# Kernel tuning notes

Hardware: AMD Instinct MI355X
Metric: run time of the kernel (lower is better)

## Reference

```python
import jax, jax.numpy as jnp
import numpy as np
from jax import lax


def _lstm_last(x, Wih, Whh, bih, bhh):
    """Single-layer torch-style LSTM (gate order i,f,g,o); returns last hidden state.
    x: (M, T, F) -> (M, H)."""
    gx = jnp.einsum('mtf,gf->mtg', x, Wih) + bih + bhh  # precompute input contributions
    H = Whh.shape[1]
    Wh = Whh.T
    def step(carry, g):
        h, c = carry
        z = g + h @ Wh
        i, f, gg, o = jnp.split(z, 4, axis=-1)
        c = jax.nn.sigmoid(f) * c + jax.nn.sigmoid(i) * jnp.tanh(gg)
        h = jax.nn.sigmoid(o) * jnp.tanh(c)
        return (h, c), None
    M = x.shape[0]
    init = (jnp.zeros((M, H), x.dtype), jnp.zeros((M, H), x.dtype))
    (h, _), _ = lax.scan(step, init, jnp.swapaxes(gx, 0, 1))
    return h


def _forward(input_data, rel_encoding, lstm_Wih, lstm_Whh, lstm_bih, lstm_bhh,
             hop_w1, hop_b1, hop_w2, hop_b2, fn_w1, fn_b1, fn_w2, fn_b2):
    B, W, N, F = input_data.shape
    U = lstm_Whh.shape[1]
    # SequentialEmbedding: per-stock LSTM over the window, take last step
    x = jnp.transpose(input_data, (0, 2, 1, 3)).reshape(B * N, W, F)
    seq = _lstm_last(x, lstm_Wih, lstm_Whh, lstm_bih, lstm_bhh).reshape(B, N, U)

    # RelationalEmbedding: dense N x N k-hop message passing
    mask = (rel_encoding.sum(-1) > 0).astype(seq.dtype)  # (N,N)
    D = mask.sum(-1)                                      # (N,) degrees (self-loops keep >0)
    e = seq
    for k in range(hop_w1.shape[0]):  # k_hops: small fixed loop
        W1 = hop_w1[k]
        # mask * concat([e_i, e_j, enc]) @ W1 + b1, computed blockwise without
        # materializing the (B,N,N,2U+K) concat; mask scales only the pre-bias term
        xi = e @ W1[:U]                                    # (B,N,INP)
        xj = e @ W1[U:2 * U]                               # (B,N,INP)
        xe = jnp.einsum('ijk,kp->ijp', rel_encoding, W1[2 * U:])  # (N,N,INP)
        pre = mask[None, :, :, None] * (xi[:, :, None, :] + xj[:, None, :, :] + xe[None]) + hop_b1[k]
        hdn = jax.nn.leaky_relu(pre)                       # (B,N,N,INP)
        wts = jax.nn.leaky_relu(hdn @ hop_w2[k] + hop_b2[k])[..., 0]  # (B,N,N)
        scaled = (wts * mask) / D[None, :, None]
        # torch: sum_i scaled[b,i,j] * e_j  ==  e_j * (sum_i scaled[b,i,j])
        e = scaled.sum(axis=1)[..., None] * e

    # FullyConnected head: Linear(2U,2U)+LeakyReLU, Linear(2U,1)+LeakyReLU, squeeze
    comb = jnp.concatenate([seq, e], axis=-1)              # (B,N,2U)
    out = jax.nn.leaky_relu(comb @ fn_w1 + fn_b1)
    out = jax.nn.leaky_relu(out @ fn_w2 + fn_b2)
    return out[..., 0]                                     # (B,N)


def setup_inputs() -> dict:
    key = jax.random.key(0)
    ks = jax.random.split(key, 14)
    B, W, N, F = 2, 32, 768, 4
    U, K, KH = 32, 8, 2
    INP = 2 * U + K  # 72
    def w(k, shape, fan):
        return jax.random.normal(k, shape, jnp.float32) / np.float32(np.sqrt(fan))
    enc = (jax.random.uniform(ks[1], (N, N, K)) < 0.05).astype(jnp.float32)
    # self-loops in relation channel 0 so every node has degree >= 1
    enc = enc.at[:, :, 0].set(jnp.maximum(enc[:, :, 0], jnp.eye(N, dtype=jnp.float32)))
    return {
        'input_data': jax.random.normal(ks[0], (B, W, N, F), jnp.float32),
        'rel_encoding': enc,
        'lstm_Wih': w(ks[2], (4 * U, F), F),
        'lstm_Whh': w(ks[3], (4 * U, U), U),
        'lstm_bih': 0.01 * jax.random.normal(ks[4], (4 * U,), jnp.float32),
        'lstm_bhh': 0.01 * jax.random.normal(ks[5], (4 * U,), jnp.float32),
        'hop_w1': w(ks[6], (KH, INP, INP), INP),
        'hop_b1': 0.01 * jax.random.normal(ks[7], (KH, INP), jnp.float32),
        'hop_w2': w(ks[8], (KH, INP, 1), INP),
        'hop_b2': 0.01 * jax.random.normal(ks[9], (KH, 1), jnp.float32),
        'fn_w1': w(ks[10], (2 * U, 2 * U), 2 * U),
        'fn_b1': 0.01 * jax.random.normal(ks[11], (2 * U,), jnp.float32),
        'fn_w2': w(ks[12], (2 * U, 1), 2 * U),
        'fn_b2': 0.01 * jax.random.normal(ks[13], (1,), jnp.float32),
    }


def reference(input_data, rel_encoding, lstm_Wih, lstm_Whh, lstm_bih, lstm_bhh,
              hop_w1, hop_b1, hop_w2, hop_b2, fn_w1, fn_b1, fn_w2, fn_b2):
    return _forward(input_data, rel_encoding, lstm_Wih, lstm_Whh, lstm_bih, lstm_bhh,
                    hop_w1, hop_b1, hop_w2, hop_b2, fn_w1, fn_b1, fn_w2, fn_b2)
```

## Files before the change

### kernel.cpp

```cpp
#include <hip/hip_runtime.h>

#define N_STK 768
#define BATCH 2
#define WIN   32
#define FEAT  4
#define UNITS 32
#define INP   72
#define CHUNK 64

__device__ __forceinline__ float lrelu(float v){ return v > 0.0f ? v : 0.01f*v; }
__device__ __forceinline__ float lanebcast(float v, int l){
    return __int_as_float(__builtin_amdgcn_readlane(__float_as_int(v), l));
}
__device__ __forceinline__ unsigned patof(const float* __restrict__ p){
    float4 a = *reinterpret_cast<const float4*>(p);
    float4 b = *reinterpret_cast<const float4*>(p + 4);
    unsigned m = 0;
    m |= (a.x != 0.0f) ? 1u   : 0u;
    m |= (a.y != 0.0f) ? 2u   : 0u;
    m |= (a.z != 0.0f) ? 4u   : 0u;
    m |= (a.w != 0.0f) ? 8u   : 0u;
    m |= (b.x != 0.0f) ? 16u  : 0u;
    m |= (b.y != 0.0f) ? 32u  : 0u;
    m |= (b.z != 0.0f) ? 64u  : 0u;
    m |= (b.w != 0.0f) ? 128u : 0u;
    return m;
}

__global__ __launch_bounds__(256) void k1_kernel(const float* __restrict__ rel,
        const float* __restrict__ x, const float* __restrict__ Wih,
        const float* __restrict__ Whh, const float* __restrict__ bih,
        const float* __restrict__ bhh, const float* __restrict__ hop_w1,
        const float* __restrict__ hop_b1,
        float* __restrict__ seq, float* __restrict__ invD, int* __restrict__ cnt,
        unsigned* __restrict__ list, float* __restrict__ lutlo, float* __restrict__ luthi,
        float* __restrict__ xi0, float* __restrict__ xj0){
    int j = blockIdx.x, tid = threadIdx.x;
    int wv = tid >> 6, lane = tid & 63;
    __shared__ float hrow[2][UNITS];

    if (wv < 2){
        int b = wv;
        int r0 = lane, r1 = 64 + lane;
        bool low = (lane < 32);
        float4 wi0 = *reinterpret_cast<const float4*>(Wih + r0*FEAT);
        float4 wi1 = *reinterpret_cast<const float4*>(Wih + r1*FEAT);
        float bb0 = bih[r0] + bhh[r0];
        float bb1 = bih[r1] + bhh[r1];
        float4 W0[8], W1[8];
        #pragma unroll
        for (int q = 0; q < 8; q++){
            W0[q] = *reinterpret_cast<const float4*>(Whh + r0*UNITS + q*4);
            W1[q] = *reinterpret_cast<const float4*>(Whh + r1*UNITS + q*4);
        }
        float4 xv = make_float4(0.f, 0.f, 0.f, 0.f);
        if (low) xv = *reinterpret_cast<const float4*>(x + ((size_t)(b*WIN + lane)*N_STK + j)*FEAT);
        float hreg = 0.0f, c = 0.0f;
        #pragma unroll 1
        for (int t = 0; t < WIN; t++){
            float xb0 = lanebcast(xv.x, t), xb1 = lanebcast(xv.y, t);
            float xb2 = lanebcast(xv.z, t), xb3 = lanebcast(xv.w, t);
            float z0a = bb0 + wi0.x*xb0 + wi0.z*xb2;
            float z0b =       wi0.y*xb1 + wi0.w*xb3;
            float z1a = bb1 + wi1.x*xb0 + wi1.z*xb2;
            float z1b =       wi1.y*xb1 + wi1.w*xb3;
            #pragma unroll
            for (int q = 0; q < 8; q++){
                float h0 = lanebcast(hreg, 32 + q*4 + 0);
                float h1 = lanebcast(hreg, 32 + q*4 + 1);
                float h2 = lanebcast(hreg, 32 + q*4 + 2);
                float h3 = lanebcast(hreg, 32 + q*4 + 3);
                z0a += W0[q].x*h0; z0b += W0[q].y*h1;
                z0a += W0[q].z*h2; z0b += W0[q].w*h3;
                z1a += W1[q].x*h0; z1b += W1[q].y*h1;
                z1a += W1[q].z*h2; z1b += W1[q].w*h3;
            }
            float z0 = z0a + z0b, z1 = z1a + z1b;
            float e0 = __expf(-z0);
            float s0 = 1.0f/(1.0f + e0);
            float sc = low ? -2.0f : -1.0f;
            float e1 = __expf(sc*z1);
            float rr = 1.0f/(1.0f + e1);
            float act = low ? (1.0f - e1)*rr : rr;
            float pa = s0*act;
            float po = __shfl_xor(pa, 32);
            c = s0*c + po;
            float e2 = __expf(-2.0f*c);
            float th = (1.0f - e2)/(1.0f + e2);
            hreg = act*th;
        }
        if (!low){
            hrow[b][lane - 32] = hreg;
            seq[((size_t)b*N_STK + j)*UNITS + (lane - 32)] = hreg;
        }
    } else if (wv == 2){
        int local = 0;
        for (int jj = lane; jj < N_STK; jj += 64){
            unsigned p = patof(rel + ((size_t)j*N_STK + jj)*8);
            local += p ? 1 : 0;
        }
        #pragma unroll
        for (int d = 32; d; d >>= 1) local += __shfl_xor(local, d);
        if (lane == 0) invD[j] = 1.0f/(float)local;
        if (j < 64){
            int m = j & 15, half = (j >> 4) & 1, k = j >> 5;
            const float* W = hop_w1 + (size_t)k*INP*INP;
            int base = 2*UNITS + (half ? 4 : 0);
            for (int p = lane; p < INP; p += 64){
                float acc = half ? 0.0f : hop_b1[k*INP + p];
                #pragma unroll
                for (int q = 0; q < 4; q++)
                    if ((m >> q) & 1) acc += W[(base + q)*INP + p];
                (half ? luthi : lutlo)[(k*16 + m)*INP + p] = acc;
            }
        }
    } else {
        unsigned char pv[12];
        int c = 0;
        #pragma unroll
        for (int r = 0; r < 12; r++){
            int i = lane*12 + r;
            unsigned p = patof(rel + ((size_t)i*N_STK + j)*8);
            pv[r] = (unsigned char)p;
            c += p ? 1 : 0;
        }
        int sc = c;
        #pragma unroll
        for (int off = 1; off < 64; off <<= 1){
            int v = __shfl_up(sc, off);
            if (lane >= off) sc += v;
        }
        int slot = sc - c;
        #pragma unroll
        for (int r = 0; r < 12; r++)
            if (pv[r]) list[(size_t)j*N_STK + (slot++)] = (unsigned)(((lane*12 + r) << 8) | pv[r]);
        int total = __shfl(sc, 63);
        if (lane == 0) cnt[j] = total;
    }
    __syncthreads();
    if (tid < 2*INP){
        int b = tid/INP, p = tid%INP;
        float si = 0.0f, sj = 0.0f;
        #pragma unroll
        for (int u = 0; u < UNITS; u++){
            float ev = hrow[b][u];
            si += ev * hop_w1[u*INP + p];
            sj += ev * hop_w1[(UNITS + u)*INP + p];
        }
        size_t o = ((size_t)b*N_STK + j)*INP + p;
        xi0[o] = si; xj0[o] = sj;
    }
}

template<int MODE>
__global__ __launch_bounds__(256) void col_kernel(const float* __restrict__ xi,
        const float* __restrict__ xj,
        const float* __restrict__ lutlo_k, const float* __restrict__ luthi_k,
        const float* __restrict__ w2, const float* __restrict__ b2,
        const unsigned* __restrict__ list, const int* __restrict__ cnt,
        const float* __restrict__ invD,
        const float* __restrict__ ein, float* __restrict__ eout,
        const float* __restrict__ W1next, float* __restrict__ xi_next, float* __restrict__ xj_next,
        const float* __restrict__ seqg, const float* __restrict__ fw1,
        const float* __restrict__ fb1, const float* __restrict__ fw2,
        const float* __restrict__ fb2, float* __restrict__ outp){
    int j = blockIdx.x, tid = threadIdx.x;
    int cn = cnt[j];
    __shared__ float xi_sh[2][CHUNK*INP];
    __shared__ float xjlo_sh[2][16*INP];
    __shared__ float hi_sh[16*INP];
    __shared__ float red[4][2];
    __shared__ float sval[2];
    __shared__ float ep_sh[2][64];
    for (int idx = tid; idx < 16*INP; idx += 256){
        float lo = lutlo_k[idx];
        xjlo_sh[0][idx] = lo + xj[((size_t)0*N_STK + j)*INP + (idx % INP)];
        xjlo_sh[1][idx] = lo + xj[((size_t)1*N_STK + j)*INP + (idx % INP)];
        hi_sh[idx] = luthi_k[idx];
    }
    int e  = tid >> 2;
    int bb = (tid >> 1) & 1;
    int hf = tid & 1;
    float4 w2h[9];
    #pragma unroll
    for (int q = 0; q < 9; q++) w2h[q] = *reinterpret_cast<const float4*>(w2 + hf*36 + q*4);
    float b2v = b2[0];
    float accb = 0.0f;

    for (int base = 0; base < cn; base += CHUNK){
        __syncthreads();
        for (int u = tid; u < CHUNK*36; u += 256){
            int eu = u / 36;
            if (base + eu < cn){
                int r = u - eu*36;
                int sb = r / 18, q = r - sb*18;
                unsigned ent = list[(size_t)j*N_STK + base + eu];
                int i = (int)(ent >> 8);
                *reinterpret_cast<float4*>(&xi_sh[sb][eu*INP + q*4]) =
                    *reinterpret_cast<const float4*>(xi + ((size_t)sb*N_STK + i)*INP + q*4);
            }
        }
        __syncthreads();
        bool alive = (base + e < cn);
        unsigned ent = alive ? list[(size_t)j*N_STK + base + e] : 0u;
        int i = (int)(ent >> 8);
        int mlo = (int)(ent & 15u), mhi = (int)((ent >> 4) & 15u);
        const float* xr = &xi_sh[bb][e*INP + hf*36];
        const float* jr = &xjlo_sh[bb][mlo*INP + hf*36];
        const float* hr = &hi_sh[mhi*INP + hf*36];
        float4 a = make_float4(0.f, 0.f, 0.f, 0.f);
        #pragma unroll
        for (int q = 0; q < 9; q++){
            float4 xv = *reinterpret_cast<const float4*>(xr + q*4);
            float4 jv = *reinterpret_cast<const float4*>(jr + q*4);
            float4 hv = *reinterpret_cast<const float4*>(hr + q*4);
            float4 w  = w2h[q];
            a.x += lrelu(xv.x + jv.x + hv.x)*w.x;
            a.y += lrelu(xv.y + jv.y + hv.y)*w.y;
            a.z += lrelu(xv.z + jv.z + hv.z)*w.z;
            a.w += lrelu(xv.w + jv.w + hv.w)*w.w;
        }
        float dot = a.x + a.y + a.z + a.w;
        dot += __shfl_xor(dot, 1);
        if (alive && hf == 0) accb += lrelu(dot + b2v)*invD[i];
    }
    #pragma unroll
    for (int d = 4; d < 64; d <<= 1) accb += __shfl_xor(accb, d);
    int lw = tid & 63, w = tid >> 6;
    if (lw == 0) red[w][0] = accb;
    if (lw == 2) red[w][1] = accb;
    __syncthreads();
    if (tid < 2) sval[tid] = red[0][tid] + red[1][tid] + red[2][tid] + red[3][tid];
    __syncthreads();

    if (tid < 64){
        int b = tid >> 5, u = tid & 31;
        size_t o = ((size_t)b*N_STK + j)*UNITS + u;
        float ev = ein[o]*sval[b];
        if (MODE == 0){
            ep_sh[b][u] = ev;
            eout[o] = ev;
        } else {
            ep_sh[b][32 + u] = ev;
            ep_sh[b][u] = seqg[o];
        }
    }
    __syncthreads();
    if (MODE == 0){
        if (tid < 2*INP){
            int b = tid/INP, p = tid%INP;
            float si = 0.0f, sj = 0.0f;
            #pragma unroll
            for (int u = 0; u < UNITS; u++){
                float ev = ep_sh[b][u];
                si += ev * W1next[u*INP + p];
                sj += ev * W1next[(UNITS + u)*INP + p];
            }
            size_t o = ((size_t)b*N_STK + j)*INP + p;
            xi_next[o] = si; xj_next[o] = sj;
        }
    } else {
        if (tid < 128){
            int b = tid >> 6, u = tid & 63;
            float acc = fb1[u];
            #pragma unroll 8
            for (int d = 0; d < 64; d++) acc += ep_sh[b][d]*fw1[d*64 + u];
            float prod = lrelu(acc)*fw2[u];
            prod += __shfl_xor(prod, 32);
            prod += __shfl_xor(prod, 16);
            prod += __shfl_xor(prod, 8);
            prod += __shfl_xor(prod, 4);
            prod += __shfl_xor(prod, 2);
            prod += __shfl_xor(prod, 1);
            if (u == 0) outp[b*N_STK + j] = lrelu(prod + fb2[0]);
        }
    }
}

extern "C" void kernel_launch(void* const* d_in, const int* in_sizes, int n_in,
                              void* d_out, int out_size, void* d_ws, size_t ws_size,
                              hipStream_t stream){
    const float* input_data = (const float*)d_in[0];
    const float* rel        = (const float*)d_in[1];
    const float* lstm_Wih   = (const float*)d_in[2];
    const float* lstm_Whh   = (const float*)d_in[3];
    const float* lstm_bih   = (const float*)d_in[4];
    const float* lstm_bhh   = (const float*)d_in[5];
    const float* hop_w1     = (const float*)d_in[6];
    const float* hop_b1     = (const float*)d_in[7];
    const float* hop_w2     = (const float*)d_in[8];
    const float* hop_b2     = (const float*)d_in[9];
    const float* fn_w1      = (const float*)d_in[10];
    const float* fn_b1      = (const float*)d_in[11];
    const float* fn_w2      = (const float*)d_in[12];
    const float* fn_b2      = (const float*)d_in[13];
    float* out = (float*)d_out;

    float* ws    = (float*)d_ws;
    float* seq   = ws;
    float* eA    = seq   + 49152;
    float* xi0   = eA    + 49152;
    float* xj0   = xi0   + 110592;
    float* xi1   = xj0   + 110592;
    float* xj1   = xi1   + 110592;
    float* lutlo = xj1   + 110592;
    float* luthi = lutlo + 2304;
    float* invD  = luthi + 2304;
    int*   cnt   = (int*)(invD + 768);
    unsigned* list = (unsigned*)(cnt + 768);

    k1_kernel<<<N_STK, 256, 0, stream>>>(rel, input_data, lstm_Wih, lstm_Whh,
            lstm_bih, lstm_bhh, hop_w1, hop_b1,
            seq, invD, cnt, list, lutlo, luthi, xi0, xj0);

    col_kernel<0><<<N_STK, 256, 0, stream>>>(xi0, xj0, lutlo, luthi,
            hop_w2, hop_b2, list, cnt, invD,
            seq, eA, hop_w1 + INP*INP, xi1, xj1,
            nullptr, nullptr, nullptr, nullptr, nullptr, nullptr);

    col_kernel<1><<<N_STK, 256, 0, stream>>>(xi1, xj1, lutlo + 16*INP, luthi + 16*INP,
            hop_w2 + INP, hop_b2 + 1, list, cnt, invD,
            eA, nullptr, nullptr, nullptr, nullptr,
            seq, fn_w1, fn_b1, fn_w2, fn_b2, out);
}
```

Before: 176.9 us.

## Split column kernel by batch and double-buffer gathers with async global-to-LDS loads

The column kernels now launch one block per (stock, batch) pair instead of one block handling both batches. Each block gathers neighbour xi rows straight into LDS with global_load_lds, double-buffered so the next chunk's gather overlaps compute on the current chunk. Rows are padded to 76 floats and each thread covers a quarter of a row. The aim is to double parallelism and hide gather latency, at the cost of redundant prologue and epilogue work per batch and padded, clamped extra loads.

```diff
diff --git a/kernel.cpp b/kernel.cpp
--- a/kernel.cpp
+++ b/kernel.cpp
@@ -7,6 +7,8 @@
 #define UNITS 32
 #define INP   72
 #define CHUNK 64
+#define LROW  76
+#define NSLC  19
 
 __device__ __forceinline__ float lrelu(float v){ return v > 0.0f ? v : 0.01f*v; }
 __device__ __forceinline__ float lanebcast(float v, int l){
@@ -25,6 +27,12 @@
     m |= (b.z != 0.0f) ? 64u  : 0u;
     m |= (b.w != 0.0f) ? 128u : 0u;
     return m;
+}
+__device__ __forceinline__ void async_cp16(const float* g, float* l){
+    __builtin_amdgcn_global_load_lds(
+        (const __attribute__((address_space(1))) unsigned int*)g,
+        (__attribute__((address_space(3))) unsigned int*)l,
+        16, 0, 0);
 }
 
 __global__ __launch_bounds__(256) void k1_kernel(const float* __restrict__ rel,
@@ -164,115 +172,144 @@
         const float* __restrict__ seqg, const float* __restrict__ fw1,
         const float* __restrict__ fb1, const float* __restrict__ fw2,
         const float* __restrict__ fb2, float* __restrict__ outp){
-    int j = blockIdx.x, tid = threadIdx.x;
+    int j = blockIdx.x, b = blockIdx.y, tid = threadIdx.x;
     int cn = cnt[j];
-    __shared__ float xi_sh[2][CHUNK*INP];
-    __shared__ float xjlo_sh[2][16*INP];
+    __shared__ float xi_buf[2][CHUNK*LROW];
+    __shared__ float xjlo_sh[16*INP];
     __shared__ float hi_sh[16*INP];
-    __shared__ float red[4][2];
-    __shared__ float sval[2];
-    __shared__ float ep_sh[2][64];
+    __shared__ float red[4];
+    __shared__ float sval;
+    __shared__ float ep_sh[64];
+
+    const float* xib = xi + (size_t)b*N_STK*INP;
+    const unsigned* ljp = list + (size_t)j*N_STK;
+
     for (int idx = tid; idx < 16*INP; idx += 256){
-        float lo = lutlo_k[idx];
-        xjlo_sh[0][idx] = lo + xj[((size_t)0*N_STK + j)*INP + (idx % INP)];
-        xjlo_sh[1][idx] = lo + xj[((size_t)1*N_STK + j)*INP + (idx % INP)];
-        hi_sh[idx] = luthi_k[idx];
-    }
-    int e  = tid >> 2;
-    int bb = (tid >> 1) & 1;
-    int hf = tid & 1;
-    float4 w2h[9];
+        xjlo_sh[idx] = lutlo_k[idx] + xj[((size_t)b*N_STK + j)*INP + (idx % INP)];
+        hi_sh[idx]   = luthi_k[idx];
+    }
+    int e4 = tid >> 2, qt = tid & 3;
+    float4 w2r[5];
     #pragma unroll
-    for (int q = 0; q < 9; q++) w2h[q] = *reinterpret_cast<const float4*>(w2 + hf*36 + q*4);
+    for (int k = 0; k < 4; k++) w2r[k] = *reinterpret_cast<const float4*>(w2 + qt*4 + 16*k);
+    w2r[4] = (qt < 2) ? *reinterpret_cast<const float4*>(w2 + 64 + qt*4)
+                      : make_float4(0.f,0.f,0.f,0.f);
     float b2v = b2[0];
+
+    int nch = (cn + CHUNK - 1)/CHUNK;
+
+    auto stage = [&](int c, int sb){
+        int base = c*CHUNK;
+        float* dst = &xi_buf[sb][0];
+        #pragma unroll
+        for (int r = 0; r < 4; r++){
+            int u = r*256 + tid;
+            int eu = u/NSLC, sl = u - eu*NSLC;
+            int idx = base + eu; if (idx > cn - 1) idx = cn - 1;
+            int i = (int)(ljp[idx] >> 8);
+            int off = (sl < 18) ? sl*4 : 0;
+            async_cp16(xib + (size_t)i*INP + off, dst + u*4);
+        }
+        {
+            int u = 1024 + tid;
+            if (u < CHUNK*NSLC){
+                int eu = u/NSLC, sl = u - eu*NSLC;
+                int idx = base + eu; if (idx > cn - 1) idx = cn - 1;
+                int i = (int)(ljp[idx] >> 8);
+                int off = (sl < 18) ? sl*4 : 0;
+                async_cp16(xib + (size_t)i*INP + off, dst + u*4);
+            }
+        }
+    };
+
+    stage(0, 0);
+    __syncthreads();
+
     float accb = 0.0f;
-
-    for (int base = 0; base < cn; base += CHUNK){
-        __syncthreads();
-        for (int u = tid; u < CHUNK*36; u += 256){
-            int eu = u / 36;
-            if (base + eu < cn){
-                int r = u - eu*36;
-                int sb = r / 18, q = r - sb*18;
-                unsigned ent = list[(size_t)j*N_STK + base + eu];
-                int i = (int)(ent >> 8);
-                *reinterpret_cast<float4*>(&xi_sh[sb][eu*INP + q*4]) =
-                    *reinterpret_cast<const float4*>(xi + ((size_t)sb*N_STK + i)*INP + q*4);
-            }
-        }
-        __syncthreads();
-        bool alive = (base + e < cn);
-        unsigned ent = alive ? list[(size_t)j*N_STK + base + e] : 0u;
+    for (int c = 0; c < nch; c++){
+        if (c + 1 < nch) stage(c + 1, (c + 1) & 1);
+        int idx = c*CHUNK + e4;
+        bool alive = idx < cn;
+        unsigned ent = ljp[alive ? idx : cn - 1];
         int i = (int)(ent >> 8);
         int mlo = (int)(ent & 15u), mhi = (int)((ent >> 4) & 15u);
-        const float* xr = &xi_sh[bb][e*INP + hf*36];
-        const float* jr = &xjlo_sh[bb][mlo*INP + hf*36];
-        const float* hr = &hi_sh[mhi*INP + hf*36];
-        float4 a = make_float4(0.f, 0.f, 0.f, 0.f);
-        #pragma unroll
-        for (int q = 0; q < 9; q++){
-            float4 xv = *reinterpret_cast<const float4*>(xr + q*4);
-            float4 jv = *reinterpret_cast<const float4*>(jr + q*4);
-            float4 hv = *reinterpret_cast<const float4*>(hr + q*4);
-            float4 w  = w2h[q];
-            a.x += lrelu(xv.x + jv.x + hv.x)*w.x;
-            a.y += lrelu(xv.y + jv.y + hv.y)*w.y;
-            a.z += lrelu(xv.z + jv.z + hv.z)*w.z;
-            a.w += lrelu(xv.w + jv.w + hv.w)*w.w;
-        }
-        float dot = a.x + a.y + a.z + a.w;
-        dot += __shfl_xor(dot, 1);
-        if (alive && hf == 0) accb += lrelu(dot + b2v)*invD[i];
+        const float* xr = &xi_buf[c & 1][e4*LROW];
+        const float* jr = &xjlo_sh[mlo*INP];
+        const float* hr = &hi_sh[mhi*INP];
+        float acc = 0.0f;
+        #pragma unroll
+        for (int k = 0; k < 4; k++){
+            int o = qt*4 + 16*k;
+            float4 xv = *reinterpret_cast<const float4*>(xr + o);
+            float4 jv = *reinterpret_cast<const float4*>(jr + o);
+            float4 hv = *reinterpret_cast<const float4*>(hr + o);
+            float4 w  = w2r[k];
+            acc += lrelu(xv.x + jv.x + hv.x)*w.x;
+            acc += lrelu(xv.y + jv.y + hv.y)*w.y;
+            acc += lrelu(xv.z + jv.z + hv.z)*w.z;
+            acc += lrelu(xv.w + jv.w + hv.w)*w.w;
+        }
+        if (qt < 2){
+            int o = 64 + qt*4;
+            float4 xv = *reinterpret_cast<const float4*>(xr + o);
+            float4 jv = *reinterpret_cast<const float4*>(jr + o);
+            float4 hv = *reinterpret_cast<const float4*>(hr + o);
+            float4 w  = w2r[4];
+            acc += lrelu(xv.x + jv.x + hv.x)*w.x;
+            acc += lrelu(xv.y + jv.y + hv.y)*w.y;
+            acc += lrelu(xv.z + jv.z + hv.z)*w.z;
+            acc += lrelu(xv.w + jv.w + hv.w)*w.w;
+        }
+        acc += __shfl_xor(acc, 1);
+        acc += __shfl_xor(acc, 2);
+        if (alive && qt == 0) accb += lrelu(acc + b2v)*invD[i];
+        __syncthreads();
     }
     #pragma unroll
-    for (int d = 4; d < 64; d <<= 1) accb += __shfl_xor(accb, d);
-    int lw = tid & 63, w = tid >> 6;
-    if (lw == 0) red[w][0] = accb;
-    if (lw == 2) red[w][1] = accb;
+    for (int d = 1; d < 64; d <<= 1) accb += __shfl_xor(accb, d);
+    if ((tid & 63) == 0) red[tid >> 6] = accb;
     __syncthreads();
-    if (tid < 2) sval[tid] = red[0][tid] + red[1][tid] + red[2][tid] + red[3][tid];
+    if (tid == 0) sval = red[0] + red[1] + red[2] + red[3];
     __syncthreads();
 
-    if (tid < 64){
-        int b = tid >> 5, u = tid & 31;
-        size_t o = ((size_t)b*N_STK + j)*UNITS + u;
-        float ev = ein[o]*sval[b];
-        if (MODE == 0){
-            ep_sh[b][u] = ev;
+    if (MODE == 0){
+        if (tid < 32){
+            size_t o = ((size_t)b*N_STK + j)*UNITS + tid;
+            float ev = ein[o]*sval;
+            ep_sh[tid] = ev;
             eout[o] = ev;
-        } else {
-            ep_sh[b][32 + u] = ev;
-            ep_sh[b][u] = seqg[o];
-        }
-    }
-    __syncthreads();
-    if (MODE == 0){
-        if (tid < 2*INP){
-            int b = tid/INP, p = tid%INP;
+        }
+        __syncthreads();
+        if (tid < INP){
             float si = 0.0f, sj = 0.0f;
             #pragma unroll
             for (int u = 0; u < UNITS; u++){
-                float ev = ep_sh[b][u];
-                si += ev * W1next[u*INP + p];
-                sj += ev * W1next[(UNITS + u)*INP + p];
+                float ev = ep_sh[u];
+                si += ev * W1next[u*INP + tid];
+                sj += ev * W1next[(UNITS + u)*INP + tid];
             }
-            size_t o = ((size_t)b*N_STK + j)*INP + p;
+            size_t o = ((size_t)b*N_STK + j)*INP + tid;
             xi_next[o] = si; xj_next[o] = sj;
         }
     } else {
-        if (tid < 128){
-            int b = tid >> 6, u = tid & 63;
-            float acc = fb1[u];
+        if (tid < 32){
+            size_t o = ((size_t)b*N_STK + j)*UNITS + tid;
+            ep_sh[32 + tid] = ein[o]*sval;
+            ep_sh[tid] = seqg[o];
+        }
+        __syncthreads();
+        if (tid < 64){
+            float acc = fb1[tid];
             #pragma unroll 8
-            for (int d = 0; d < 64; d++) acc += ep_sh[b][d]*fw1[d*64 + u];
-            float prod = lrelu(acc)*fw2[u];
+            for (int d = 0; d < 64; d++) acc += ep_sh[d]*fw1[d*64 + tid];
+            float prod = lrelu(acc)*fw2[tid];
             prod += __shfl_xor(prod, 32);
             prod += __shfl_xor(prod, 16);
             prod += __shfl_xor(prod, 8);
             prod += __shfl_xor(prod, 4);
             prod += __shfl_xor(prod, 2);
             prod += __shfl_xor(prod, 1);
-            if (u == 0) outp[b*N_STK + j] = lrelu(prod + fb2[0]);
+            if (tid == 0) outp[b*N_STK + j] = lrelu(prod + fb2[0]);
         }
     }
 }
@@ -313,12 +350,13 @@
             lstm_bih, lstm_bhh, hop_w1, hop_b1,
             seq, invD, cnt, list, lutlo, luthi, xi0, xj0);
 
-    col_kernel<0><<<N_STK, 256, 0, stream>>>(xi0, xj0, lutlo, luthi,
+    dim3 cgrid(N_STK, BATCH);
+    col_kernel<0><<<cgrid, 256, 0, stream>>>(xi0, xj0, lutlo, luthi,
             hop_w2, hop_b2, list, cnt, invD,
             seq, eA, hop_w1 + INP*INP, xi1, xj1,
             nullptr, nullptr, nullptr, nullptr, nullptr, nullptr);
 
-    col_kernel<1><<<N_STK, 256, 0, stream>>>(xi1, xj1, lutlo + 16*INP, luthi + 16*INP,
+    col_kernel<1><<<cgrid, 256, 0, stream>>>(xi1, xj1, lutlo + 16*INP, luthi + 16*INP,
             hop_w2 + INP, hop_b2 + 1, list, cnt, invD,
             eA, nullptr, nullptr, nullptr, nullptr,
             seq, fn_w1, fn_b1, fn_w2, fn_b2, out);
```

Result: faster. 168.2 us (-4.9%).

## Restructure column kernel to stream full xi tiles shared across column groups

Applied to the files above, without the earlier changes.

Each block now handles three columns for one batch element (grid N/3 x B). It streams all xi rows in 128-row phases into LDS with async global-to-LDS copies, instead of gathering only neighbor rows per column. Binary search on the sorted neighbor list finds each column's edges per phase, and edges of all three columns are processed together. This is meant to replace scattered gathers with coalesced bulk loads and reuse each xi tile across columns, at the cost of loading non-neighbor rows and adding phase barriers.

```diff
diff --git a/kernel.cpp b/kernel.cpp
--- a/kernel.cpp
+++ b/kernel.cpp
@@ -6,7 +6,11 @@
 #define FEAT  4
 #define UNITS 32
 #define INP   72
-#define CHUNK 64
+#define GCOL  3
+#define NPH   6
+#define PROWS 128
+#define LROW  76
+#define NSLC  19
 
 __device__ __forceinline__ float lrelu(float v){ return v > 0.0f ? v : 0.01f*v; }
 __device__ __forceinline__ float lanebcast(float v, int l){
@@ -25,6 +29,12 @@
     m |= (b.z != 0.0f) ? 64u  : 0u;
     m |= (b.w != 0.0f) ? 128u : 0u;
     return m;
+}
+__device__ __forceinline__ void async_cp16(const float* g, float* l){
+    __builtin_amdgcn_global_load_lds(
+        (const __attribute__((address_space(1))) unsigned int*)g,
+        (__attribute__((address_space(3))) unsigned int*)l,
+        16, 0, 0);
 }
 
 __global__ __launch_bounds__(256) void k1_kernel(const float* __restrict__ rel,
@@ -164,107 +174,143 @@
         const float* __restrict__ seqg, const float* __restrict__ fw1,
         const float* __restrict__ fb1, const float* __restrict__ fw2,
         const float* __restrict__ fb2, float* __restrict__ outp){
-    int j = blockIdx.x, tid = threadIdx.x;
-    int cn = cnt[j];
-    __shared__ float xi_sh[2][CHUNK*INP];
-    __shared__ float xjlo_sh[2][16*INP];
-    __shared__ float hi_sh[16*INP];
-    __shared__ float red[4][2];
-    __shared__ float sval[2];
-    __shared__ float ep_sh[2][64];
-    for (int idx = tid; idx < 16*INP; idx += 256){
-        float lo = lutlo_k[idx];
-        xjlo_sh[0][idx] = lo + xj[((size_t)0*N_STK + j)*INP + (idx % INP)];
-        xjlo_sh[1][idx] = lo + xj[((size_t)1*N_STK + j)*INP + (idx % INP)];
-        hi_sh[idx] = luthi_k[idx];
-    }
-    int e  = tid >> 2;
-    int bb = (tid >> 1) & 1;
-    int hf = tid & 1;
-    float4 w2h[9];
+    int g = blockIdx.x, b = blockIdx.y, tid = threadIdx.x;
+    int j0 = g*GCOL;
+    __shared__ float xi_sh[PROWS*LROW];
+    __shared__ float lo_sh[16*LROW];
+    __shared__ float hi_sh[16*LROW];
+    __shared__ float xj_sh[GCOL*LROW];
+    __shared__ int   bnd_sh[GCOL][NPH+1];
+    __shared__ float red_sh[GCOL][4];
+    __shared__ float sval[GCOL];
+    __shared__ float ep_sh[GCOL][64];
+
+    const float* xib = xi + (size_t)b*N_STK*INP;
+
+    for (int idx = tid; idx < 16*18; idx += 256){
+        int m = idx/18, q = (idx - m*18)*4;
+        *reinterpret_cast<float4*>(&lo_sh[m*LROW + q]) = *reinterpret_cast<const float4*>(lutlo_k + m*INP + q);
+        *reinterpret_cast<float4*>(&hi_sh[m*LROW + q]) = *reinterpret_cast<const float4*>(luthi_k + m*INP + q);
+    }
+    if (tid < GCOL*18){
+        int c = tid/18, q = (tid - c*18)*4;
+        *reinterpret_cast<float4*>(&xj_sh[c*LROW + q]) =
+            *reinterpret_cast<const float4*>(xj + ((size_t)b*N_STK + j0 + c)*INP + q);
+    }
+    if (tid < GCOL*(NPH+1)){
+        int c = tid/(NPH+1), ph = tid - c*(NPH+1);
+        const unsigned* lj = list + (size_t)(j0+c)*N_STK;
+        int lo = 0, hi = cnt[j0+c];
+        int thr = ph*PROWS;
+        while (lo < hi){ int md = (lo+hi)>>1; if ((int)(lj[md]>>8) < thr) lo = md+1; else hi = md; }
+        bnd_sh[c][ph] = lo;
+    }
+
+    int e2 = tid >> 1, hf = tid & 1;
+    float4 w2r[9];
     #pragma unroll
-    for (int q = 0; q < 9; q++) w2h[q] = *reinterpret_cast<const float4*>(w2 + hf*36 + q*4);
+    for (int q = 0; q < 9; q++) w2r[q] = *reinterpret_cast<const float4*>(w2 + hf*36 + q*4);
     float b2v = b2[0];
-    float accb = 0.0f;
-
-    for (int base = 0; base < cn; base += CHUNK){
+    float acc0 = 0.0f, acc1 = 0.0f, acc2 = 0.0f;
+
+    for (int ph = 0; ph < NPH; ph++){
+        #pragma unroll
+        for (int it = 0; it < 10; it++){
+            int u = it*256 + tid;
+            if (u < PROWS*NSLC){
+                int row = u/NSLC, sl = u - row*NSLC;
+                int off = (sl < 18) ? sl*4 : 0;
+                async_cp16(xib + (size_t)(ph*PROWS + row)*INP + off, &xi_sh[0] + (size_t)u*4);
+            }
+        }
         __syncthreads();
-        for (int u = tid; u < CHUNK*36; u += 256){
-            int eu = u / 36;
-            if (base + eu < cn){
-                int r = u - eu*36;
-                int sb = r / 18, q = r - sb*18;
-                unsigned ent = list[(size_t)j*N_STK + base + eu];
-                int i = (int)(ent >> 8);
-                *reinterpret_cast<float4*>(&xi_sh[sb][eu*INP + q*4]) =
-                    *reinterpret_cast<const float4*>(xi + ((size_t)sb*N_STK + i)*INP + q*4);
+
+        int c0b = bnd_sh[0][ph], c0n = bnd_sh[0][ph+1] - c0b;
+        int c1b = bnd_sh[1][ph], c1n = bnd_sh[1][ph+1] - c1b;
+        int c2b = bnd_sh[2][ph], c2n = bnd_sh[2][ph+1] - c2b;
+        int off1 = c0n, off2 = c0n + c1n, tot = off2 + c2n;
+        for (int gsl = e2; gsl < tot; gsl += 128){
+            int c, e;
+            if (gsl < off1){ c = 0; e = c0b + gsl; }
+            else if (gsl < off2){ c = 1; e = c1b + (gsl - off1); }
+            else { c = 2; e = c2b + (gsl - off2); }
+            unsigned ent = list[(size_t)(j0+c)*N_STK + e];
+            int ig = (int)(ent >> 8);
+            int mlo = (int)(ent & 15u), mhi = (int)((ent >> 4) & 15u);
+            const float* xr = &xi_sh[(ig - ph*PROWS)*LROW + hf*36];
+            const float* jr = &xj_sh[c*LROW + hf*36];
+            const float* lr = &lo_sh[mlo*LROW + hf*36];
+            const float* hr = &hi_sh[mhi*LROW + hf*36];
+            float dot = 0.0f;
+            #pragma unroll
+            for (int q = 0; q < 9; q++){
+                float4 xv = *reinterpret_cast<const float4*>(xr + q*4);
+                float4 jv = *reinterpret_cast<const float4*>(jr + q*4);
+                float4 lv = *reinterpret_cast<const float4*>(lr + q*4);
+                float4 hv = *reinterpret_cast<const float4*>(hr + q*4);
+                float4 w  = w2r[q];
+                dot += lrelu(xv.x + jv.x + lv.x + hv.x)*w.x;
+                dot += lrelu(xv.y + jv.y + lv.y + hv.y)*w.y;
+                dot += lrelu(xv.z + jv.z + lv.z + hv.z)*w.z;
+                dot += lrelu(xv.w + jv.w + lv.w + hv.w)*w.w;
+            }
+            dot += __shfl_xor(dot, 1);
+            if (hf == 0){
+                float v = lrelu(dot + b2v)*invD[ig];
+                acc0 += (c == 0) ? v : 0.0f;
+                acc1 += (c == 1) ? v : 0.0f;
+                acc2 += (c == 2) ? v : 0.0f;
             }
         }
         __syncthreads();
-        bool alive = (base + e < cn);
-        unsigned ent = alive ? list[(size_t)j*N_STK + base + e] : 0u;
-        int i = (int)(ent >> 8);
-        int mlo = (int)(ent & 15u), mhi = (int)((ent >> 4) & 15u);
-        const float* xr = &xi_sh[bb][e*INP + hf*36];
-        const float* jr = &xjlo_sh[bb][mlo*INP + hf*36];
-        const float* hr = &hi_sh[mhi*INP + hf*36];
-        float4 a = make_float4(0.f, 0.f, 0.f, 0.f);
-        #pragma unroll
-        for (int q = 0; q < 9; q++){
-            float4 xv = *reinterpret_cast<const float4*>(xr + q*4);
-            float4 jv = *reinterpret_cast<const float4*>(jr + q*4);
-            float4 hv = *reinterpret_cast<const float4*>(hr + q*4);
-            float4 w  = w2h[q];
-            a.x += lrelu(xv.x + jv.x + hv.x)*w.x;
-            a.y += lrelu(xv.y + jv.y + hv.y)*w.y;
-            a.z += lrelu(xv.z + jv.z + hv.z)*w.z;
-            a.w += lrelu(xv.w + jv.w + hv.w)*w.w;
-        }
-        float dot = a.x + a.y + a.z + a.w;
-        dot += __shfl_xor(dot, 1);
-        if (alive && hf == 0) accb += lrelu(dot + b2v)*invD[i];
-    }
+    }
+
     #pragma unroll
-    for (int d = 4; d < 64; d <<= 1) accb += __shfl_xor(accb, d);
-    int lw = tid & 63, w = tid >> 6;
-    if (lw == 0) red[w][0] = accb;
-    if (lw == 2) red[w][1] = accb;
+    for (int d = 1; d < 64; d <<= 1){
+        acc0 += __shfl_xor(acc0, d);
+        acc1 += __shfl_xor(acc1, d);
+        acc2 += __shfl_xor(acc2, d);
+    }
+    int w = tid >> 6;
+    if ((tid & 63) == 0){ red_sh[0][w] = acc0; red_sh[1][w] = acc1; red_sh[2][w] = acc2; }
     __syncthreads();
-    if (tid < 2) sval[tid] = red[0][tid] + red[1][tid] + red[2][tid] + red[3][tid];
+    if (tid < GCOL) sval[tid] = red_sh[tid][0] + red_sh[tid][1] + red_sh[tid][2] + red_sh[tid][3];
     __syncthreads();
 
-    if (tid < 64){
-        int b = tid >> 5, u = tid & 31;
-        size_t o = ((size_t)b*N_STK + j)*UNITS + u;
-        float ev = ein[o]*sval[b];
-        if (MODE == 0){
-            ep_sh[b][u] = ev;
+    if (MODE == 0){
+        if (tid < GCOL*32){
+            int c = tid >> 5, u = tid & 31;
+            size_t o = ((size_t)b*N_STK + j0 + c)*UNITS + u;
+            float ev = ein[o]*sval[c];
+            ep_sh[c][u] = ev;
             eout[o] = ev;
-        } else {
-            ep_sh[b][32 + u] = ev;
-            ep_sh[b][u] = seqg[o];
-        }
-    }
-    __syncthreads();
-    if (MODE == 0){
-        if (tid < 2*INP){
-            int b = tid/INP, p = tid%INP;
+        }
+        __syncthreads();
+        if (tid < GCOL*INP){
+            int c = tid/INP, p = tid - c*INP;
             float si = 0.0f, sj = 0.0f;
             #pragma unroll
             for (int u = 0; u < UNITS; u++){
-                float ev = ep_sh[b][u];
+                float ev = ep_sh[c][u];
                 si += ev * W1next[u*INP + p];
                 sj += ev * W1next[(UNITS + u)*INP + p];
             }
-            size_t o = ((size_t)b*N_STK + j)*INP + p;
+            size_t o = ((size_t)b*N_STK + j0 + c)*INP + p;
             xi_next[o] = si; xj_next[o] = sj;
         }
     } else {
-        if (tid < 128){
-            int b = tid >> 6, u = tid & 63;
+        if (tid < GCOL*32){
+            int c = tid >> 5, u = tid & 31;
+            size_t o = ((size_t)b*N_STK + j0 + c)*UNITS + u;
+            ep_sh[c][32 + u] = ein[o]*sval[c];
+            ep_sh[c][u] = seqg[o];
+        }
+        __syncthreads();
+        if (tid < GCOL*64){
+            int c = tid >> 6, u = tid & 63;
             float acc = fb1[u];
             #pragma unroll 8
-            for (int d = 0; d < 64; d++) acc += ep_sh[b][d]*fw1[d*64 + u];
+            for (int d = 0; d < 64; d++) acc += ep_sh[c][d]*fw1[d*64 + u];
             float prod = lrelu(acc)*fw2[u];
             prod += __shfl_xor(prod, 32);
             prod += __shfl_xor(prod, 16);
@@ -272,7 +318,7 @@
             prod += __shfl_xor(prod, 4);
             prod += __shfl_xor(prod, 2);
             prod += __shfl_xor(prod, 1);
-            if (u == 0) outp[b*N_STK + j] = lrelu(prod + fb2[0]);
+            if (u == 0) outp[b*N_STK + j0 + c] = lrelu(prod + fb2[0]);
         }
     }
 }
@@ -313,12 +359,13 @@
             lstm_bih, lstm_bhh, hop_w1, hop_b1,
             seq, invD, cnt, list, lutlo, luthi, xi0, xj0);
 
-    col_kernel<0><<<N_STK, 256, 0, stream>>>(xi0, xj0, lutlo, luthi,
+    dim3 cgrid(N_STK/GCOL, BATCH);
+    col_kernel<0><<<cgrid, 256, 0, stream>>>(xi0, xj0, lutlo, luthi,
             hop_w2, hop_b2, list, cnt, invD,
             seq, eA, hop_w1 + INP*INP, xi1, xj1,
             nullptr, nullptr, nullptr, nullptr, nullptr, nullptr);
 
-    col_kernel<1><<<N_STK, 256, 0, stream>>>(xi1, xj1, lutlo + 16*INP, luthi + 16*INP,
+    col_kernel<1><<<cgrid, 256, 0, stream>>>(xi1, xj1, lutlo + 16*INP, luthi + 16*INP,
             hop_w2 + INP, hop_b2 + 1, list, cnt, invD,
             eA, nullptr, nullptr, nullptr, nullptr,
             seq, fn_w1, fn_b1, fn_w2, fn_b2, out);
```

Result: faster. 166.9 us (-5.7%).

## Tile hop message passing over i×j blocks with dense pattern bytes and atomics

Applied to the files above, without the earlier changes.

Replaces the per-column edge-list gather with a 2D tiled hop kernel. Each block takes a 64-row by 24-column tile of the N×N mask, stages xi, xj and the LUT rows in LDS through async global-to-LDS copies, and builds a local edge list from a dense byte pattern matrix. Partial column sums are combined with shared and global atomics. The epilogue moves into separate ep kernels, which adds two launches and requires zeroing the global accumulators, and float atomics make the summation order nondeterministic.

```diff
diff --git a/kernel.cpp b/kernel.cpp
--- a/kernel.cpp
+++ b/kernel.cpp
@@ -6,7 +6,12 @@
 #define FEAT  4
 #define UNITS 32
 #define INP   72
-#define CHUNK 64
+#define LROW  76
+#define NSLC  19
+#define IPH   64
+#define JCR   24
+#define NPHI  12
+#define NCR   32
 
 __device__ __forceinline__ float lrelu(float v){ return v > 0.0f ? v : 0.01f*v; }
 __device__ __forceinline__ float lanebcast(float v, int l){
@@ -26,18 +31,27 @@
     m |= (b.w != 0.0f) ? 128u : 0u;
     return m;
 }
+__device__ __forceinline__ void async_cp16(const float* g, float* l){
+    __builtin_amdgcn_global_load_lds(
+        (const __attribute__((address_space(1))) unsigned int*)g,
+        (__attribute__((address_space(3))) unsigned int*)l,
+        16, 0, 0);
+}
 
 __global__ __launch_bounds__(256) void k1_kernel(const float* __restrict__ rel,
         const float* __restrict__ x, const float* __restrict__ Wih,
         const float* __restrict__ Whh, const float* __restrict__ bih,
         const float* __restrict__ bhh, const float* __restrict__ hop_w1,
         const float* __restrict__ hop_b1,
-        float* __restrict__ seq, float* __restrict__ invD, int* __restrict__ cnt,
-        unsigned* __restrict__ list, float* __restrict__ lutlo, float* __restrict__ luthi,
-        float* __restrict__ xi0, float* __restrict__ xj0){
+        float* __restrict__ seq, float* __restrict__ invD,
+        unsigned char* __restrict__ Pout,
+        float* __restrict__ lutlo, float* __restrict__ luthi,
+        float* __restrict__ xi0, float* __restrict__ xj0,
+        float* __restrict__ s0){
     int j = blockIdx.x, tid = threadIdx.x;
     int wv = tid >> 6, lane = tid & 63;
     __shared__ float hrow[2][UNITS];
+    __shared__ int cw_sh[2];
 
     if (wv < 2){
         int b = wv;
@@ -77,14 +91,14 @@
             }
             float z0 = z0a + z0b, z1 = z1a + z1b;
             float e0 = __expf(-z0);
-            float s0 = 1.0f/(1.0f + e0);
+            float s0g = 1.0f/(1.0f + e0);
             float sc = low ? -2.0f : -1.0f;
             float e1 = __expf(sc*z1);
             float rr = 1.0f/(1.0f + e1);
             float act = low ? (1.0f - e1)*rr : rr;
-            float pa = s0*act;
+            float pa = s0g*act;
             float po = __shfl_xor(pa, 32);
-            c = s0*c + po;
+            c = s0g*c + po;
             float e2 = __expf(-2.0f*c);
             float th = (1.0f - e2)/(1.0f + e2);
             hreg = act*th;
@@ -93,53 +107,38 @@
             hrow[b][lane - 32] = hreg;
             seq[((size_t)b*N_STK + j)*UNITS + (lane - 32)] = hreg;
         }
-    } else if (wv == 2){
+    } else {
+        int half = wv - 2;
         int local = 0;
-        for (int jj = lane; jj < N_STK; jj += 64){
-            unsigned p = patof(rel + ((size_t)j*N_STK + jj)*8);
+        #pragma unroll
+        for (int k = 0; k < 6; k++){
+            int col = half*384 + k*64 + lane;
+            unsigned p = patof(rel + ((size_t)j*N_STK + col)*8);
+            Pout[(size_t)j*N_STK + col] = (unsigned char)p;
             local += p ? 1 : 0;
         }
         #pragma unroll
         for (int d = 32; d; d >>= 1) local += __shfl_xor(local, d);
-        if (lane == 0) invD[j] = 1.0f/(float)local;
-        if (j < 64){
-            int m = j & 15, half = (j >> 4) & 1, k = j >> 5;
-            const float* W = hop_w1 + (size_t)k*INP*INP;
-            int base = 2*UNITS + (half ? 4 : 0);
-            for (int p = lane; p < INP; p += 64){
-                float acc = half ? 0.0f : hop_b1[k*INP + p];
-                #pragma unroll
-                for (int q = 0; q < 4; q++)
-                    if ((m >> q) & 1) acc += W[(base + q)*INP + p];
-                (half ? luthi : lutlo)[(k*16 + m)*INP + p] = acc;
-            }
-        }
-    } else {
-        unsigned char pv[12];
-        int c = 0;
-        #pragma unroll
-        for (int r = 0; r < 12; r++){
-            int i = lane*12 + r;
-            unsigned p = patof(rel + ((size_t)i*N_STK + j)*8);
-            pv[r] = (unsigned char)p;
-            c += p ? 1 : 0;
-        }
-        int sc = c;
-        #pragma unroll
-        for (int off = 1; off < 64; off <<= 1){
-            int v = __shfl_up(sc, off);
-            if (lane >= off) sc += v;
-        }
-        int slot = sc - c;
-        #pragma unroll
-        for (int r = 0; r < 12; r++)
-            if (pv[r]) list[(size_t)j*N_STK + (slot++)] = (unsigned)(((lane*12 + r) << 8) | pv[r]);
-        int total = __shfl(sc, 63);
-        if (lane == 0) cnt[j] = total;
-    }
-    __syncthreads();
+        if (lane == 0) cw_sh[half] = local;
+    }
+    __syncthreads();
+    if (tid == 0){
+        invD[j] = 1.0f/(float)(cw_sh[0] + cw_sh[1]);
+        s0[j] = 0.0f; s0[N_STK + j] = 0.0f;
+    }
+    if (j < 64 && tid >= 144 && tid < 216){
+        int p = tid - 144;
+        int m = j & 15, half = (j >> 4) & 1, k = j >> 5;
+        const float* W = hop_w1 + (size_t)k*INP*INP;
+        float acc = half ? 0.0f : hop_b1[k*INP + p];
+        int base = 2*UNITS + (half ? 4 : 0);
+        #pragma unroll
+        for (int q = 0; q < 4; q++)
+            if ((m >> q) & 1) acc += W[(base + q)*INP + p];
+        (half ? luthi : lutlo)[(k*16 + m)*INP + p] = acc;
+    }
     if (tid < 2*INP){
-        int b = tid/INP, p = tid%INP;
+        int b = tid/INP, p = tid - b*INP;
         float si = 0.0f, sj = 0.0f;
         #pragma unroll
         for (int u = 0; u < UNITS; u++){
@@ -152,107 +151,130 @@
     }
 }
 
-template<int MODE>
-__global__ __launch_bounds__(256) void col_kernel(const float* __restrict__ xi,
+__global__ __launch_bounds__(256) void hop_kernel(const float* __restrict__ xi,
         const float* __restrict__ xj,
         const float* __restrict__ lutlo_k, const float* __restrict__ luthi_k,
         const float* __restrict__ w2, const float* __restrict__ b2,
-        const unsigned* __restrict__ list, const int* __restrict__ cnt,
-        const float* __restrict__ invD,
-        const float* __restrict__ ein, float* __restrict__ eout,
-        const float* __restrict__ W1next, float* __restrict__ xi_next, float* __restrict__ xj_next,
-        const float* __restrict__ seqg, const float* __restrict__ fw1,
-        const float* __restrict__ fb1, const float* __restrict__ fw2,
-        const float* __restrict__ fb2, float* __restrict__ outp){
-    int j = blockIdx.x, tid = threadIdx.x;
-    int cn = cnt[j];
-    __shared__ float xi_sh[2][CHUNK*INP];
-    __shared__ float xjlo_sh[2][16*INP];
-    __shared__ float hi_sh[16*INP];
-    __shared__ float red[4][2];
-    __shared__ float sval[2];
-    __shared__ float ep_sh[2][64];
-    for (int idx = tid; idx < 16*INP; idx += 256){
-        float lo = lutlo_k[idx];
-        xjlo_sh[0][idx] = lo + xj[((size_t)0*N_STK + j)*INP + (idx % INP)];
-        xjlo_sh[1][idx] = lo + xj[((size_t)1*N_STK + j)*INP + (idx % INP)];
-        hi_sh[idx] = luthi_k[idx];
-    }
-    int e  = tid >> 2;
-    int bb = (tid >> 1) & 1;
+        const unsigned char* __restrict__ P, const float* __restrict__ invD,
+        float* __restrict__ s_out){
+    int cr = blockIdx.x, ip = blockIdx.y, b = blockIdx.z;
+    int j0 = cr*JCR, i0 = ip*IPH, tid = threadIdx.x;
+    __shared__ float xi_sh[IPH*LROW];
+    __shared__ float xj_sh[JCR*LROW];
+    __shared__ float lo_sh[16*LROW];
+    __shared__ float hi_sh[16*LROW];
+    __shared__ float invD_sh[IPH];
+    __shared__ float acc_sh[JCR];
+    __shared__ unsigned elist[IPH*JCR];
+    __shared__ int lcnt;
+
+    const float* xib = xi + ((size_t)b*N_STK + i0)*INP;
+    const float* xjb = xj + ((size_t)b*N_STK + j0)*INP;
+
+    if (tid == 0) lcnt = 0;
+    if (tid < JCR) acc_sh[tid] = 0.0f;
+    __syncthreads();
+
+    for (int u = tid; u < IPH*NSLC; u += 256){
+        int r = u/NSLC, sl = u - r*NSLC;
+        int off = (sl < 18) ? sl*4 : 0;
+        async_cp16(xib + (size_t)r*INP + off, &xi_sh[0] + (size_t)u*4);
+    }
+    for (int u = tid; u < JCR*NSLC; u += 256){
+        int r = u/NSLC, sl = u - r*NSLC;
+        int off = (sl < 18) ? sl*4 : 0;
+        async_cp16(xjb + (size_t)r*INP + off, &xj_sh[0] + (size_t)u*4);
+    }
+    for (int u = tid; u < 16*NSLC; u += 256){
+        int r = u/NSLC, sl = u - r*NSLC;
+        int off = (sl < 18) ? sl*4 : 0;
+        async_cp16(lutlo_k + r*INP + off, &lo_sh[0] + (size_t)u*4);
+    }
+    for (int u = tid; u < 16*NSLC; u += 256){
+        int r = u/NSLC, sl = u - r*NSLC;
+        int off = (sl < 18) ? sl*4 : 0;
+        async_cp16(luthi_k + r*INP + off, &hi_sh[0] + (size_t)u*4);
+    }
+    if (tid < IPH/4) async_cp16(invD + i0 + tid*4, &invD_sh[0] + tid*4);
+
+    if (tid < IPH){
+        const unsigned* prow = reinterpret_cast<const unsigned*>(P + (size_t)(i0 + tid)*N_STK + j0);
+        unsigned w[6];
+        #pragma unroll
+        for (int k = 0; k < 6; k++) w[k] = prow[k];
+        #pragma unroll
+        for (int k = 0; k < 24; k++){
+            unsigned pat = (w[k >> 2] >> ((k & 3)*8)) & 255u;
+            if (pat){
+                int pos = atomicAdd(&lcnt, 1);
+                elist[pos] = ((unsigned)tid << 13) | ((unsigned)k << 8) | pat;
+            }
+        }
+    }
+
     int hf = tid & 1;
-    float4 w2h[9];
+    float4 w2r[9];
     #pragma unroll
-    for (int q = 0; q < 9; q++) w2h[q] = *reinterpret_cast<const float4*>(w2 + hf*36 + q*4);
+    for (int q = 0; q < 9; q++) w2r[q] = *reinterpret_cast<const float4*>(w2 + hf*36 + q*4);
     float b2v = b2[0];
-    float accb = 0.0f;
-
-    for (int base = 0; base < cn; base += CHUNK){
-        __syncthreads();
-        for (int u = tid; u < CHUNK*36; u += 256){
-            int eu = u / 36;
-            if (base + eu < cn){
-                int r = u - eu*36;
-                int sb = r / 18, q = r - sb*18;
-                unsigned ent = list[(size_t)j*N_STK + base + eu];
-                int i = (int)(ent >> 8);
-                *reinterpret_cast<float4*>(&xi_sh[sb][eu*INP + q*4]) =
-                    *reinterpret_cast<const float4*>(xi + ((size_t)sb*N_STK + i)*INP + q*4);
-            }
-        }
-        __syncthreads();
-        bool alive = (base + e < cn);
-        unsigned ent = alive ? list[(size_t)j*N_STK + base + e] : 0u;
-        int i = (int)(ent >> 8);
+    __syncthreads();
+
+    int m = lcnt;
+    for (int sl = tid >> 1; sl < m; sl += 128){
+        unsigned ent = elist[sl];
+        int il = ent >> 13, jl = (ent >> 8) & 31;
         int mlo = (int)(ent & 15u), mhi = (int)((ent >> 4) & 15u);
-        const float* xr = &xi_sh[bb][e*INP + hf*36];
-        const float* jr = &xjlo_sh[bb][mlo*INP + hf*36];
-        const float* hr = &hi_sh[mhi*INP + hf*36];
-        float4 a = make_float4(0.f, 0.f, 0.f, 0.f);
+        const float* xr = &xi_sh[il*LROW + hf*36];
+        const float* jr = &xj_sh[jl*LROW + hf*36];
+        const float* lr = &lo_sh[mlo*LROW + hf*36];
+        const float* hr = &hi_sh[mhi*LROW + hf*36];
+        float dot = 0.0f;
         #pragma unroll
         for (int q = 0; q < 9; q++){
             float4 xv = *reinterpret_cast<const float4*>(xr + q*4);
             float4 jv = *reinterpret_cast<const float4*>(jr + q*4);
+            float4 lv = *reinterpret_cast<const float4*>(lr + q*4);
             float4 hv = *reinterpret_cast<const float4*>(hr + q*4);
-            float4 w  = w2h[q];
-            a.x += lrelu(xv.x + jv.x + hv.x)*w.x;
-            a.y += lrelu(xv.y + jv.y + hv.y)*w.y;
-            a.z += lrelu(xv.z + jv.z + hv.z)*w.z;
-            a.w += lrelu(xv.w + jv.w + hv.w)*w.w;
-        }
-        float dot = a.x + a.y + a.z + a.w;
+            float4 w  = w2r[q];
+            dot += lrelu(xv.x + jv.x + lv.x + hv.x)*w.x;
+            dot += lrelu(xv.y + jv.y + lv.y + hv.y)*w.y;
+            dot += lrelu(xv.z + jv.z + lv.z + hv.z)*w.z;
+            dot += lrelu(xv.w + jv.w + lv.w + hv.w)*w.w;
+        }
         dot += __shfl_xor(dot, 1);
-        if (alive && hf == 0) accb += lrelu(dot + b2v)*invD[i];
-    }
-    #pragma unroll
-    for (int d = 4; d < 64; d <<= 1) accb += __shfl_xor(accb, d);
-    int lw = tid & 63, w = tid >> 6;
-    if (lw == 0) red[w][0] = accb;
-    if (lw == 2) red[w][1] = accb;
-    __syncthreads();
-    if (tid < 2) sval[tid] = red[0][tid] + red[1][tid] + red[2][tid] + red[3][tid];
-    __syncthreads();
-
+        if (hf == 0) atomicAdd(&acc_sh[jl], lrelu(dot + b2v)*invD_sh[il]);
+    }
+    __syncthreads();
+    if (tid < JCR) atomicAdd(&s_out[b*N_STK + j0 + tid], acc_sh[tid]);
+}
+
+template<int MODE>
+__global__ __launch_bounds__(192) void ep_kernel(const float* __restrict__ sview,
+        const float* __restrict__ ein, const float* __restrict__ seqg,
+        float* __restrict__ eout,
+        const float* __restrict__ W1next, float* __restrict__ xi_next,
+        float* __restrict__ xj_next, float* __restrict__ s_next,
+        const float* __restrict__ fw1, const float* __restrict__ fb1,
+        const float* __restrict__ fw2, const float* __restrict__ fb2,
+        float* __restrict__ outp){
+    int j = blockIdx.x, tid = threadIdx.x;
+    __shared__ float e_sh[2][64];
     if (tid < 64){
         int b = tid >> 5, u = tid & 31;
         size_t o = ((size_t)b*N_STK + j)*UNITS + u;
-        float ev = ein[o]*sval[b];
-        if (MODE == 0){
-            ep_sh[b][u] = ev;
-            eout[o] = ev;
-        } else {
-            ep_sh[b][32 + u] = ev;
-            ep_sh[b][u] = seqg[o];
-        }
-    }
+        float ev = ein[o]*sview[b*N_STK + j];
+        if (MODE == 0){ e_sh[b][u] = ev; eout[o] = ev; }
+        else          { e_sh[b][32 + u] = ev; e_sh[b][u] = seqg[o]; }
+    }
+    if (MODE == 0 && tid >= 160 && tid < 162) s_next[(tid - 160)*N_STK + j] = 0.0f;
     __syncthreads();
     if (MODE == 0){
         if (tid < 2*INP){
-            int b = tid/INP, p = tid%INP;
+            int b = tid/INP, p = tid - b*INP;
             float si = 0.0f, sj = 0.0f;
             #pragma unroll
             for (int u = 0; u < UNITS; u++){
-                float ev = ep_sh[b][u];
+                float ev = e_sh[b][u];
                 si += ev * W1next[u*INP + p];
                 sj += ev * W1next[(UNITS + u)*INP + p];
             }
@@ -264,7 +286,7 @@
             int b = tid >> 6, u = tid & 63;
             float acc = fb1[u];
             #pragma unroll 8
-            for (int d = 0; d < 64; d++) acc += ep_sh[b][d]*fw1[d*64 + u];
+            for (int d = 0; d < 64; d++) acc += e_sh[b][d]*fw1[d*64 + u];
             float prod = lrelu(acc)*fw2[u];
             prod += __shfl_xor(prod, 32);
             prod += __shfl_xor(prod, 16);
@@ -306,20 +328,26 @@
     float* lutlo = xj1   + 110592;
     float* luthi = lutlo + 2304;
     float* invD  = luthi + 2304;
-    int*   cnt   = (int*)(invD + 768);
-    unsigned* list = (unsigned*)(cnt + 768);
+    float* s0    = invD  + 768;
+    float* s1    = s0    + 1536;
+    unsigned char* P = (unsigned char*)(s1 + 1536);
 
     k1_kernel<<<N_STK, 256, 0, stream>>>(rel, input_data, lstm_Wih, lstm_Whh,
             lstm_bih, lstm_bhh, hop_w1, hop_b1,
-            seq, invD, cnt, list, lutlo, luthi, xi0, xj0);
-
-    col_kernel<0><<<N_STK, 256, 0, stream>>>(xi0, xj0, lutlo, luthi,
-            hop_w2, hop_b2, list, cnt, invD,
-            seq, eA, hop_w1 + INP*INP, xi1, xj1,
-            nullptr, nullptr, nullptr, nullptr, nullptr, nullptr);
-
-    col_kernel<1><<<N_STK, 256, 0, stream>>>(xi1, xj1, lutlo + 16*INP, luthi + 16*INP,
-            hop_w2 + INP, hop_b2 + 1, list, cnt, invD,
-            eA, nullptr, nullptr, nullptr, nullptr,
-            seq, fn_w1, fn_b1, fn_w2, fn_b2, out);
-}
+            seq, invD, P, lutlo, luthi, xi0, xj0, s0);
+
+    dim3 hgrid(NCR, NPHI, BATCH);
+    hop_kernel<<<hgrid, 256, 0, stream>>>(xi0, xj0, lutlo, luthi,
+            hop_w2, hop_b2, P, invD, s0);
+
+    ep_kernel<0><<<N_STK, 192, 0, stream>>>(s0, seq, nullptr, eA,
+            hop_w1 + INP*INP, xi1, xj1, s1,
+            nullptr, nullptr, nullptr, nullptr, nullptr);
+
+    hop_kernel<<<hgrid, 256, 0, stream>>>(xi1, xj1, lutlo + 16*INP, luthi + 16*INP,
+            hop_w2 + INP, hop_b2 + 1, P, invD, s1);
+
+    ep_kernel<1><<<N_STK, 192, 0, stream>>>(s1, eA, seq, nullptr,
+            nullptr, nullptr, nullptr, nullptr,
+            fn_w1, fn_b1, fn_w2, fn_b2, out);
+}
```

After: 148.6 us. -16.0%, faster.
